# Kernel tuning notes

Hardware: AMD Instinct MI355X
Metric: run time of the kernel (lower is better)

The kernel has to match this reference:

```python
import jax, jax.numpy as jnp
import numpy as np

NUM_USERS, NUM_ITEMS, NUM_GROUPS = 100000, 50000, 20000
D = 64
B, M = 16384, 50


def setup_inputs() -> dict:
    key = jax.random.key(0)
    ks = jax.random.split(key, 16)
    inp = {
        "group_inputs": jax.random.randint(ks[0], (B,), 0, NUM_GROUPS),
        "item_inputs": jax.random.randint(ks[1], (B,), 0, NUM_ITEMS),
        "member_ids": jax.random.randint(ks[2], (B, M), 0, NUM_USERS),
        "member_lengths": jax.random.randint(ks[3], (B,), 0, M),
        # embedding tables (xavier-ish scale)
        "user_table": jax.random.normal(ks[4], (NUM_USERS, D), jnp.float32) * 0.05,
        "item_table": jax.random.normal(ks[5], (NUM_ITEMS, D), jnp.float32) * 0.05,
        "group_table": jax.random.normal(ks[6], (NUM_GROUPS, D), jnp.float32) * 0.05,
        # attention MLP: 2D -> 16 -> 1
        "att_w1": jax.random.normal(ks[7], (2 * D, 16), jnp.float32) * 0.1,
        "att_b1": jnp.zeros((16,), jnp.float32),
        "att_w2": jax.random.normal(ks[8], (16, 1), jnp.float32) * 0.1,
        "att_b2": jnp.zeros((1,), jnp.float32),
        # predict MLP: 3D -> 8 -> 1
        "pred_w1": jax.random.normal(ks[9], (3 * D, 8), jnp.float32) * 0.1,
        "pred_b1": jnp.zeros((8,), jnp.float32),
        "pred_w2": jax.random.normal(ks[10], (8, 1), jnp.float32) * 0.1,
        "pred_b2": jnp.zeros((1,), jnp.float32),
    }
    return inp


def reference(group_inputs, item_inputs, member_ids, member_lengths,
              user_table, item_table, group_table,
              att_w1, att_b1, att_w2, att_b2,
              pred_w1, pred_b1, pred_w2, pred_b2):
    # mask: at least one valid member per group
    mask = jnp.arange(M)[None, :] <= member_lengths[:, None]          # [B, M] bool
    mem_e = user_table[member_ids]                                    # [B, M, D]
    item_e = item_table[item_inputs]                                  # [B, D]

    # attention over members: concat(member, item) -> 16 -> 1
    gi = jnp.concatenate(
        [mem_e, jnp.broadcast_to(item_e[:, None, :], mem_e.shape)], axis=-1)  # [B, M, 2D]
    h = jax.nn.relu(jnp.einsum('bmk,kh->bmh', gi, att_w1) + att_b1)   # [B, M, 16]
    scores = (jnp.einsum('bmh,ho->bmo', h, att_w2) + att_b2)[..., 0]  # [B, M]
    scores = jnp.where(mask, scores, -jnp.inf)
    at_wt = jax.nn.softmax(scores, axis=-1)                           # [B, M]

    g_att = jnp.einsum('bm,bmd->bd', at_wt, mem_e)                    # [B, D]
    g = g_att + group_table[group_inputs]                             # [B, D]

    elem = g * item_e
    new_e = jnp.concatenate([elem, g, item_e], axis=-1)               # [B, 3D]
    ph = jax.nn.relu(new_e @ pred_w1 + pred_b1)                       # [B, 8]
    y = jax.nn.sigmoid(ph @ pred_w2 + pred_b2)                        # [B, 1]
    return y
```

## Files before the change

kernel.cpp:

```cpp
#include <hip/hip_runtime.h>
#include <math.h>

constexpr int MM = 50;
constexpr int DD = 64;
constexpr int HH = 16;
constexpr int PH = 8;
constexpr int WAVES_PER_BLOCK = 4;
constexpr int SLOTS = 56;

__device__ __forceinline__ unsigned bf16rne(float f) {
    const unsigned u = __float_as_uint(f);
    return (u + 0x7FFFu + ((u >> 16) & 1u)) >> 16;
}

__global__ __launch_bounds__(256) void precompute_kernel(
    const float* __restrict__ user_table,
    const float* __restrict__ item_table,
    const int*   __restrict__ item_inputs,
    const float* __restrict__ att_w1,
    const float* __restrict__ att_b1,
    unsigned short* __restrict__ Ubf,
    float* __restrict__ Ib,
    unsigned short* __restrict__ Ub,
    int nU, int B, int userBlocks)
{
    const bool isU = (int)blockIdx.x < userBlocks;
    const float4* rp;
    const float*  w1;
    float acc[HH];
    int row = 0;

    if (isU) {
        row = (int)blockIdx.x * 256 + (int)threadIdx.x;
        if (row >= nU) return;
        rp  = (const float4*)(user_table + (size_t)row * DD);
        w1  = att_w1;
        #pragma unroll
        for (int j = 0; j < HH; ++j) acc[j] = 0.0f;
    } else {
        row = ((int)blockIdx.x - userBlocks) * 256 + (int)threadIdx.x;
        if (row >= B) return;
        const int item = item_inputs[row];
        rp  = (const float4*)(item_table + (size_t)item * DD);
        w1  = att_w1 + (size_t)DD * HH;
        #pragma unroll
        for (int j = 0; j < HH; ++j) acc[j] = att_b1[j];
    }

    unsigned brow[DD / 2];

    #pragma unroll 4
    for (int d4 = 0; d4 < DD / 4; ++d4) {
        const float4 x = rp[d4];
        const float* w = w1 + (size_t)(d4 * 4) * HH;
        #pragma unroll
        for (int j = 0; j < HH; ++j) {
            acc[j] = fmaf(x.x, w[0 * HH + j], acc[j]);
            acc[j] = fmaf(x.y, w[1 * HH + j], acc[j]);
            acc[j] = fmaf(x.z, w[2 * HH + j], acc[j]);
            acc[j] = fmaf(x.w, w[3 * HH + j], acc[j]);
        }
        brow[2 * d4]     = bf16rne(x.x) | (bf16rne(x.y) << 16);
        brow[2 * d4 + 1] = bf16rne(x.z) | (bf16rne(x.w) << 16);
    }

    if (isU) {
        unsigned uw[8];
        #pragma unroll
        for (int w = 0; w < 8; ++w)
            uw[w] = bf16rne(acc[2 * w]) | (bf16rne(acc[2 * w + 1]) << 16);
        uint4* u4 = (uint4*)(Ubf + (size_t)row * HH);
        u4[0] = make_uint4(uw[0], uw[1], uw[2], uw[3]);
        u4[1] = make_uint4(uw[4], uw[5], uw[6], uw[7]);

        uint4* b4 = (uint4*)(Ub + (size_t)row * DD);
        #pragma unroll
        for (int i = 0; i < DD / 8; ++i)
            b4[i] = make_uint4(brow[4 * i], brow[4 * i + 1],
                               brow[4 * i + 2], brow[4 * i + 3]);
    } else {
        float4* o4 = (float4*)(Ib + (size_t)row * HH);
        o4[0] = make_float4(acc[0],  acc[1],  acc[2],  acc[3]);
        o4[1] = make_float4(acc[4],  acc[5],  acc[6],  acc[7]);
        o4[2] = make_float4(acc[8],  acc[9],  acc[10], acc[11]);
        o4[3] = make_float4(acc[12], acc[13], acc[14], acc[15]);
    }
}

__global__ __launch_bounds__(256) void agree_main(
    const int* __restrict__ group_inputs,
    const int* __restrict__ item_inputs,
    const int* __restrict__ member_ids,
    const int* __restrict__ member_lengths,
    const float* __restrict__ item_table,
    const float* __restrict__ group_table,
    const float* __restrict__ att_w2,
    const float* __restrict__ att_b2,
    const float* __restrict__ pred_w1,
    const float* __restrict__ pred_b1,
    const float* __restrict__ pred_w2,
    const float* __restrict__ pred_b2,
    const unsigned short* __restrict__ Ubf,
    const float* __restrict__ Ib,
    const unsigned short* __restrict__ Ub,
    float* __restrict__ out,
    int B)
{
    __shared__ float2 pairs[WAVES_PER_BLOCK][SLOTS];

    const int lane = threadIdx.x & 63;
    const int wv   = threadIdx.x >> 6;
    const int b    = blockIdx.x * WAVES_PER_BLOCK + wv;
    if (b >= B) return;

    const int my_m  = (lane < MM) ? lane : (MM - 1);
    const int my_id = member_ids[b * MM + my_m];
    const int len   = member_lengths[b];
    const int item_idx = item_inputs[b];
    const int gid      = group_inputs[b];

    const float item_d = item_table[(unsigned)(item_idx * DD + lane)];
    const float grp_d  = group_table[(unsigned)(gid * DD + lane)];

    const uint4* up = (const uint4*)(Ubf + ((size_t)(unsigned)my_id * HH));
    const uint4 ua = up[0], ubw = up[1];
    const float* ib = Ib + (size_t)b * HH;

    float score = att_b2[0];
    {
        const unsigned uw[8] = { ua.x, ua.y, ua.z, ua.w,
                                 ubw.x, ubw.y, ubw.z, ubw.w };
        #pragma unroll
        for (int w = 0; w < 8; ++w) {
            const float f0 = __uint_as_float(uw[w] << 16);
            const float f1 = __uint_as_float(uw[w] & 0xFFFF0000u);
            score = fmaf(fmaxf(f0 + ib[2 * w],     0.0f), att_w2[2 * w],     score);
            score = fmaf(fmaxf(f1 + ib[2 * w + 1], 0.0f), att_w2[2 * w + 1], score);
        }
    }

    const bool valid = (lane < MM) && (lane <= len);
    score = valid ? score : -INFINITY;

    float mx = score;
    #pragma unroll
    for (int off = 32; off > 0; off >>= 1) mx = fmaxf(mx, __shfl_xor(mx, off, 64));
    const float e = valid ? __expf(score - mx) : 0.0f;
    float sum = e;
    #pragma unroll
    for (int off = 32; off > 0; off >>= 1) sum += __shfl_xor(sum, off, 64);
    const float wnorm = e / sum;

    if (lane < SLOTS) pairs[wv][lane] = make_float2(wnorm, __int_as_float(my_id));
    __builtin_amdgcn_s_waitcnt(0);

    const int mcnt   = (len < MM - 1 ? len : MM - 1) + 1;
    const int chunks = (mcnt + 7) >> 3;

    float g = 0.0f;
    for (int c = 0; c < chunks; ++c) {
        float2 q[8];
        #pragma unroll
        for (int k = 0; k < 8; ++k) q[k] = pairs[wv][c * 8 + k];
        unsigned short xb[8];
        #pragma unroll
        for (int k = 0; k < 8; ++k) {
            const unsigned idx = (unsigned)(__float_as_int(q[k].y) * DD + lane);
            xb[k] = Ub[idx];
        }
        #pragma unroll
        for (int k = 0; k < 8; ++k)
            g = fmaf(q[k].x, __uint_as_float((unsigned)xb[k] << 16), g);
    }
    g += grp_d;

    const float elem = g * item_d;
    float p[PH];
    {
        const float* pa = pred_w1 + (size_t)lane * PH;
        const float* pb = pred_w1 + (size_t)(DD + lane) * PH;
        const float* pc = pred_w1 + (size_t)(2 * DD + lane) * PH;
        #pragma unroll
        for (int j = 0; j < PH; ++j)
            p[j] = fmaf(elem, pa[j], fmaf(g, pb[j], item_d * pc[j]));
    }
    #pragma unroll
    for (int off = 32; off > 0; off >>= 1) {
        #pragma unroll
        for (int j = 0; j < PH; ++j) p[j] += __shfl_xor(p[j], off, 64);
    }

    if (lane == 0) {
        float acc = pred_b2[0];
        #pragma unroll
        for (int j = 0; j < PH; ++j)
            acc = fmaf(fmaxf(p[j] + pred_b1[j], 0.0f), pred_w2[j], acc);
        out[b] = 1.0f / (1.0f + __expf(-acc));
    }
}

__global__ __launch_bounds__(256) void agree_fallback(
    const int* __restrict__ group_inputs,
    const int* __restrict__ item_inputs,
    const int* __restrict__ member_ids,
    const int* __restrict__ member_lengths,
    const float* __restrict__ user_table,
    const float* __restrict__ item_table,
    const float* __restrict__ group_table,
    const float* __restrict__ att_w1,
    const float* __restrict__ att_b1,
    const float* __restrict__ att_w2,
    const float* __restrict__ att_b2,
    const float* __restrict__ pred_w1,
    const float* __restrict__ pred_b1,
    const float* __restrict__ pred_w2,
    const float* __restrict__ pred_b2,
    float* __restrict__ out,
    int B)
{
    __shared__ float lds_wt[4][MM];
    __shared__ int   lds_id[4][MM];

    const int lane = threadIdx.x & 63;
    const int wave = threadIdx.x >> 6;
    const int b = blockIdx.x * 4 + wave;
    if (b >= B) return;

    const int my_m = (lane < MM) ? lane : (MM - 1);
    const int my_id = member_ids[b * MM + my_m];
    if (lane < MM) lds_id[wave][lane] = my_id;

    const int item_idx = item_inputs[b];
    const float item_d = item_table[(size_t)item_idx * DD + lane];

    float h[HH];
    {
        const float* w1row = att_w1 + (size_t)(DD + lane) * HH;
        #pragma unroll
        for (int j = 0; j < HH; ++j) h[j] = item_d * w1row[j];
        #pragma unroll
        for (int off = 32; off > 0; off >>= 1) {
            #pragma unroll
            for (int j = 0; j < HH; ++j) h[j] += __shfl_xor(h[j], off, 64);
        }
        #pragma unroll
        for (int j = 0; j < HH; ++j) h[j] += att_b1[j];
    }

    const float* myrow = user_table + (size_t)my_id * DD;
    #pragma unroll 4
    for (int d4 = 0; d4 < DD / 4; ++d4) {
        const float4 x = ((const float4*)myrow)[d4];
        const float* w1d = att_w1 + (size_t)(d4 * 4) * HH;
        #pragma unroll
        for (int j = 0; j < HH; ++j) {
            h[j] = fmaf(x.x, w1d[0 * HH + j], h[j]);
            h[j] = fmaf(x.y, w1d[1 * HH + j], h[j]);
            h[j] = fmaf(x.z, w1d[2 * HH + j], h[j]);
            h[j] = fmaf(x.w, w1d[3 * HH + j], h[j]);
        }
    }

    float score = att_b2[0];
    #pragma unroll
    for (int j = 0; j < HH; ++j) score = fmaf(fmaxf(h[j], 0.0f), att_w2[j], score);

    const int len = member_lengths[b];
    const bool valid = (lane < MM) && (lane <= len);
    score = valid ? score : -INFINITY;

    float mx = score;
    #pragma unroll
    for (int off = 32; off > 0; off >>= 1) mx = fmaxf(mx, __shfl_xor(mx, off, 64));
    float e = valid ? __expf(score - mx) : 0.0f;
    float sum = e;
    #pragma unroll
    for (int off = 32; off > 0; off >>= 1) sum += __shfl_xor(sum, off, 64);
    if (lane < MM) lds_wt[wave][lane] = e / sum;
    __builtin_amdgcn_s_waitcnt(0);

    const int mcnt = (len < MM - 1 ? len : MM - 1) + 1;
    float g = 0.0f;
    #pragma unroll 2
    for (int m = 0; m < mcnt; ++m) {
        g = fmaf(lds_wt[wave][m],
                 user_table[(size_t)lds_id[wave][m] * DD + lane], g);
    }
    const int gid = group_inputs[b];
    g += group_table[(size_t)gid * DD + lane];

    const float elem = g * item_d;
    float p[PH];
    {
        const float* pa = pred_w1 + (size_t)lane * PH;
        const float* pb = pred_w1 + (size_t)(DD + lane) * PH;
        const float* pc = pred_w1 + (size_t)(2 * DD + lane) * PH;
        #pragma unroll
        for (int j = 0; j < PH; ++j)
            p[j] = fmaf(elem, pa[j], fmaf(g, pb[j], item_d * pc[j]));
    }
    #pragma unroll
    for (int off = 32; off > 0; off >>= 1) {
        #pragma unroll
        for (int j = 0; j < PH; ++j) p[j] += __shfl_xor(p[j], off, 64);
    }

    if (lane == 0) {
        float acc = pred_b2[0];
        #pragma unroll
        for (int j = 0; j < PH; ++j)
            acc = fmaf(fmaxf(p[j] + pred_b1[j], 0.0f), pred_w2[j], acc);
        out[b] = 1.0f / (1.0f + __expf(-acc));
    }
}

extern "C" void kernel_launch(void* const* d_in, const int* in_sizes, int n_in,
                              void* d_out, int out_size, void* d_ws, size_t ws_size,
                              hipStream_t stream) {
    const int*   group_inputs   = (const int*)d_in[0];
    const int*   item_inputs    = (const int*)d_in[1];
    const int*   member_ids     = (const int*)d_in[2];
    const int*   member_lengths = (const int*)d_in[3];
    const float* user_table     = (const float*)d_in[4];
    const float* item_table     = (const float*)d_in[5];
    const float* group_table    = (const float*)d_in[6];
    const float* att_w1         = (const float*)d_in[7];
    const float* att_b1         = (const float*)d_in[8];
    const float* att_w2         = (const float*)d_in[9];
    const float* att_b2         = (const float*)d_in[10];
    const float* pred_w1        = (const float*)d_in[11];
    const float* pred_b1        = (const float*)d_in[12];
    const float* pred_w2        = (const float*)d_in[13];
    const float* pred_b2        = (const float*)d_in[14];
    float* out = (float*)d_out;

    const int B  = in_sizes[0];
    const int nU = in_sizes[4] / DD;
    const size_t need = (size_t)nU * HH * sizeof(unsigned short)
                      + (size_t)B  * HH * sizeof(float)
                      + (size_t)nU * DD * sizeof(unsigned short);
    const int blocks = (B + WAVES_PER_BLOCK - 1) / WAVES_PER_BLOCK;

    if (ws_size >= need) {
        unsigned short* Ubf = (unsigned short*)d_ws;
        float* Ib = (float*)(Ubf + (size_t)nU * HH);
        unsigned short* Ub = (unsigned short*)(Ib + (size_t)B * HH);
        const int userBlocks = (nU + 255) / 256;
        const int itemBlocks = (B + 255) / 256;
        precompute_kernel<<<userBlocks + itemBlocks, 256, 0, stream>>>(
            user_table, item_table, item_inputs, att_w1, att_b1,
            Ubf, Ib, Ub, nU, B, userBlocks);
        agree_main<<<blocks, 256, 0, stream>>>(
            group_inputs, item_inputs, member_ids, member_lengths,
            item_table, group_table,
            att_w2, att_b2, pred_w1, pred_b1, pred_w2, pred_b2,
            Ubf, Ib, Ub, out, B);
    } else {
        agree_fallback<<<blocks, 256, 0, stream>>>(
            group_inputs, item_inputs, member_ids, member_lengths,
            user_table, item_table, group_table,
            att_w1, att_b1, att_w2, att_b2,
            pred_w1, pred_b1, pred_w2, pred_b2,
            out, B);
    }
}
```

Before: 143.1 us.

## Fuse precompute into single kernel staging member rows as bf16 in LDS

Drops the separate precompute pass that projected the whole user table and wrote bf16 copies to workspace. Each lane now loads its member's fp32 row once, computes the attention hidden layer directly, and stores a bf16 copy into padded LDS. The weighted member sum then reads from LDS instead of re-gathering from global memory. This removes a full-table pass and a second gather, at the cost of more per-lane FMA work and large LDS use that may reduce occupancy.

Measured after the change: 187.9 us. +31.3%, slower.

```diff
diff --git a/kernel.cpp b/kernel.cpp
--- a/kernel.cpp
+++ b/kernel.cpp
@@ -7,199 +7,14 @@
 constexpr int PH = 8;
 constexpr int WAVES_PER_BLOCK = 4;
 constexpr int SLOTS = 56;
+constexpr int USTRIDE = 33;
 
 __device__ __forceinline__ unsigned bf16rne(float f) {
     const unsigned u = __float_as_uint(f);
     return (u + 0x7FFFu + ((u >> 16) & 1u)) >> 16;
 }
 
-__global__ __launch_bounds__(256) void precompute_kernel(
-    const float* __restrict__ user_table,
-    const float* __restrict__ item_table,
-    const int*   __restrict__ item_inputs,
-    const float* __restrict__ att_w1,
-    const float* __restrict__ att_b1,
-    unsigned short* __restrict__ Ubf,
-    float* __restrict__ Ib,
-    unsigned short* __restrict__ Ub,
-    int nU, int B, int userBlocks)
-{
-    const bool isU = (int)blockIdx.x < userBlocks;
-    const float4* rp;
-    const float*  w1;
-    float acc[HH];
-    int row = 0;
-
-    if (isU) {
-        row = (int)blockIdx.x * 256 + (int)threadIdx.x;
-        if (row >= nU) return;
-        rp  = (const float4*)(user_table + (size_t)row * DD);
-        w1  = att_w1;
-        #pragma unroll
-        for (int j = 0; j < HH; ++j) acc[j] = 0.0f;
-    } else {
-        row = ((int)blockIdx.x - userBlocks) * 256 + (int)threadIdx.x;
-        if (row >= B) return;
-        const int item = item_inputs[row];
-        rp  = (const float4*)(item_table + (size_t)item * DD);
-        w1  = att_w1 + (size_t)DD * HH;
-        #pragma unroll
-        for (int j = 0; j < HH; ++j) acc[j] = att_b1[j];
-    }
-
-    unsigned brow[DD / 2];
-
-    #pragma unroll 4
-    for (int d4 = 0; d4 < DD / 4; ++d4) {
-        const float4 x = rp[d4];
-        const float* w = w1 + (size_t)(d4 * 4) * HH;
-        #pragma unroll
-        for (int j = 0; j < HH; ++j) {
-            acc[j] = fmaf(x.x, w[0 * HH + j], acc[j]);
-            acc[j] = fmaf(x.y, w[1 * HH + j], acc[j]);
-            acc[j] = fmaf(x.z, w[2 * HH + j], acc[j]);
-            acc[j] = fmaf(x.w, w[3 * HH + j], acc[j]);
-        }
-        brow[2 * d4]     = bf16rne(x.x) | (bf16rne(x.y) << 16);
-        brow[2 * d4 + 1] = bf16rne(x.z) | (bf16rne(x.w) << 16);
-    }
-
-    if (isU) {
-        unsigned uw[8];
-        #pragma unroll
-        for (int w = 0; w < 8; ++w)
-            uw[w] = bf16rne(acc[2 * w]) | (bf16rne(acc[2 * w + 1]) << 16);
-        uint4* u4 = (uint4*)(Ubf + (size_t)row * HH);
-        u4[0] = make_uint4(uw[0], uw[1], uw[2], uw[3]);
-        u4[1] = make_uint4(uw[4], uw[5], uw[6], uw[7]);
-
-        uint4* b4 = (uint4*)(Ub + (size_t)row * DD);
-        #pragma unroll
-        for (int i = 0; i < DD / 8; ++i)
-            b4[i] = make_uint4(brow[4 * i], brow[4 * i + 1],
-                               brow[4 * i + 2], brow[4 * i + 3]);
-    } else {
-        float4* o4 = (float4*)(Ib + (size_t)row * HH);
-        o4[0] = make_float4(acc[0],  acc[1],  acc[2],  acc[3]);
-        o4[1] = make_float4(acc[4],  acc[5],  acc[6],  acc[7]);
-        o4[2] = make_float4(acc[8],  acc[9],  acc[10], acc[11]);
-        o4[3] = make_float4(acc[12], acc[13], acc[14], acc[15]);
-    }
-}
-
-__global__ __launch_bounds__(256) void agree_main(
-    const int* __restrict__ group_inputs,
-    const int* __restrict__ item_inputs,
-    const int* __restrict__ member_ids,
-    const int* __restrict__ member_lengths,
-    const float* __restrict__ item_table,
-    const float* __restrict__ group_table,
-    const float* __restrict__ att_w2,
-    const float* __restrict__ att_b2,
-    const float* __restrict__ pred_w1,
-    const float* __restrict__ pred_b1,
-    const float* __restrict__ pred_w2,
-    const float* __restrict__ pred_b2,
-    const unsigned short* __restrict__ Ubf,
-    const float* __restrict__ Ib,
-    const unsigned short* __restrict__ Ub,
-    float* __restrict__ out,
-    int B)
-{
-    __shared__ float2 pairs[WAVES_PER_BLOCK][SLOTS];
-
-    const int lane = threadIdx.x & 63;
-    const int wv   = threadIdx.x >> 6;
-    const int b    = blockIdx.x * WAVES_PER_BLOCK + wv;
-    if (b >= B) return;
-
-    const int my_m  = (lane < MM) ? lane : (MM - 1);
-    const int my_id = member_ids[b * MM + my_m];
-    const int len   = member_lengths[b];
-    const int item_idx = item_inputs[b];
-    const int gid      = group_inputs[b];
-
-    const float item_d = item_table[(unsigned)(item_idx * DD + lane)];
-    const float grp_d  = group_table[(unsigned)(gid * DD + lane)];
-
-    const uint4* up = (const uint4*)(Ubf + ((size_t)(unsigned)my_id * HH));
-    const uint4 ua = up[0], ubw = up[1];
-    const float* ib = Ib + (size_t)b * HH;
-
-    float score = att_b2[0];
-    {
-        const unsigned uw[8] = { ua.x, ua.y, ua.z, ua.w,
-                                 ubw.x, ubw.y, ubw.z, ubw.w };
-        #pragma unroll
-        for (int w = 0; w < 8; ++w) {
-            const float f0 = __uint_as_float(uw[w] << 16);
-            const float f1 = __uint_as_float(uw[w] & 0xFFFF0000u);
-            score = fmaf(fmaxf(f0 + ib[2 * w],     0.0f), att_w2[2 * w],     score);
-            score = fmaf(fmaxf(f1 + ib[2 * w + 1], 0.0f), att_w2[2 * w + 1], score);
-        }
-    }
-
-    const bool valid = (lane < MM) && (lane <= len);
-    score = valid ? score : -INFINITY;
-
-    float mx = score;
-    #pragma unroll
-    for (int off = 32; off > 0; off >>= 1) mx = fmaxf(mx, __shfl_xor(mx, off, 64));
-    const float e = valid ? __expf(score - mx) : 0.0f;
-    float sum = e;
-    #pragma unroll
-    for (int off = 32; off > 0; off >>= 1) sum += __shfl_xor(sum, off, 64);
-    const float wnorm = e / sum;
-
-    if (lane < SLOTS) pairs[wv][lane] = make_float2(wnorm, __int_as_float(my_id));
-    __builtin_amdgcn_s_waitcnt(0);
-
-    const int mcnt   = (len < MM - 1 ? len : MM - 1) + 1;
-    const int chunks = (mcnt + 7) >> 3;
-
-    float g = 0.0f;
-    for (int c = 0; c < chunks; ++c) {
-        float2 q[8];
-        #pragma unroll
-        for (int k = 0; k < 8; ++k) q[k] = pairs[wv][c * 8 + k];
-        unsigned short xb[8];
-        #pragma unroll
-        for (int k = 0; k < 8; ++k) {
-            const unsigned idx = (unsigned)(__float_as_int(q[k].y) * DD + lane);
-            xb[k] = Ub[idx];
-        }
-        #pragma unroll
-        for (int k = 0; k < 8; ++k)
-            g = fmaf(q[k].x, __uint_as_float((unsigned)xb[k] << 16), g);
-    }
-    g += grp_d;
-
-    const float elem = g * item_d;
-    float p[PH];
-    {
-        const float* pa = pred_w1 + (size_t)lane * PH;
-        const float* pb = pred_w1 + (size_t)(DD + lane) * PH;
-        const float* pc = pred_w1 + (size_t)(2 * DD + lane) * PH;
-        #pragma unroll
-        for (int j = 0; j < PH; ++j)
-            p[j] = fmaf(elem, pa[j], fmaf(g, pb[j], item_d * pc[j]));
-    }
-    #pragma unroll
-    for (int off = 32; off > 0; off >>= 1) {
-        #pragma unroll
-        for (int j = 0; j < PH; ++j) p[j] += __shfl_xor(p[j], off, 64);
-    }
-
-    if (lane == 0) {
-        float acc = pred_b2[0];
-        #pragma unroll
-        for (int j = 0; j < PH; ++j)
-            acc = fmaf(fmaxf(p[j] + pred_b1[j], 0.0f), pred_w2[j], acc);
-        out[b] = 1.0f / (1.0f + __expf(-acc));
-    }
-}
-
-__global__ __launch_bounds__(256) void agree_fallback(
+__global__ __launch_bounds__(256) void agree_fused(
     const int* __restrict__ group_inputs,
     const int* __restrict__ item_inputs,
     const int* __restrict__ member_ids,
@@ -218,76 +33,95 @@
     float* __restrict__ out,
     int B)
 {
-    __shared__ float lds_wt[4][MM];
-    __shared__ int   lds_id[4][MM];
+    __shared__ unsigned lds_u[WAVES_PER_BLOCK][SLOTS][USTRIDE];
+    __shared__ float    lds_w[WAVES_PER_BLOCK][SLOTS];
 
     const int lane = threadIdx.x & 63;
-    const int wave = threadIdx.x >> 6;
-    const int b = blockIdx.x * 4 + wave;
+    const int wv   = threadIdx.x >> 6;
+    const int b    = blockIdx.x * WAVES_PER_BLOCK + wv;
     if (b >= B) return;
 
-    const int my_m = (lane < MM) ? lane : (MM - 1);
+    const int my_m  = (lane < MM) ? lane : (MM - 1);
     const int my_id = member_ids[b * MM + my_m];
-    if (lane < MM) lds_id[wave][lane] = my_id;
+    const int len      = member_lengths[b];
+    const int item_idx = item_inputs[b];
+    const int gid      = group_inputs[b];
 
-    const int item_idx = item_inputs[b];
     const float item_d = item_table[(size_t)item_idx * DD + lane];
+    const float grp_d  = group_table[(size_t)gid * DD + lane];
 
-    float h[HH];
+    float s[HH];
     {
-        const float* w1row = att_w1 + (size_t)(DD + lane) * HH;
+        const float* w1b = att_w1 + (size_t)(DD + lane) * HH;
         #pragma unroll
-        for (int j = 0; j < HH; ++j) h[j] = item_d * w1row[j];
+        for (int j = 0; j < HH; ++j) s[j] = item_d * w1b[j];
         #pragma unroll
         for (int off = 32; off > 0; off >>= 1) {
             #pragma unroll
-            for (int j = 0; j < HH; ++j) h[j] += __shfl_xor(h[j], off, 64);
+            for (int j = 0; j < HH; ++j) s[j] += __shfl_xor(s[j], off, 64);
         }
         #pragma unroll
-        for (int j = 0; j < HH; ++j) h[j] += att_b1[j];
+        for (int j = 0; j < HH; ++j) s[j] += att_b1[j];
     }
 
-    const float* myrow = user_table + (size_t)my_id * DD;
+    const float4* myrow = (const float4*)(user_table + (size_t)(unsigned)my_id * DD);
     #pragma unroll 4
     for (int d4 = 0; d4 < DD / 4; ++d4) {
-        const float4 x = ((const float4*)myrow)[d4];
-        const float* w1d = att_w1 + (size_t)(d4 * 4) * HH;
+        const float4 x = myrow[d4];
+        const float* w = att_w1 + (size_t)(d4 * 4) * HH;
         #pragma unroll
         for (int j = 0; j < HH; ++j) {
-            h[j] = fmaf(x.x, w1d[0 * HH + j], h[j]);
-            h[j] = fmaf(x.y, w1d[1 * HH + j], h[j]);
-            h[j] = fmaf(x.z, w1d[2 * HH + j], h[j]);
-            h[j] = fmaf(x.w, w1d[3 * HH + j], h[j]);
+            s[j] = fmaf(x.x, w[0 * HH + j], s[j]);
+            s[j] = fmaf(x.y, w[1 * HH + j], s[j]);
+            s[j] = fmaf(x.z, w[2 * HH + j], s[j]);
+            s[j] = fmaf(x.w, w[3 * HH + j], s[j]);
+        }
+        if (lane < SLOTS) {
+            lds_u[wv][lane][2 * d4]     = bf16rne(x.x) | (bf16rne(x.y) << 16);
+            lds_u[wv][lane][2 * d4 + 1] = bf16rne(x.z) | (bf16rne(x.w) << 16);
         }
     }
 
     float score = att_b2[0];
     #pragma unroll
-    for (int j = 0; j < HH; ++j) score = fmaf(fmaxf(h[j], 0.0f), att_w2[j], score);
+    for (int j = 0; j < HH; ++j)
+        score = fmaf(fmaxf(s[j], 0.0f), att_w2[j], score);
 
-    const int len = member_lengths[b];
     const bool valid = (lane < MM) && (lane <= len);
     score = valid ? score : -INFINITY;
 
     float mx = score;
     #pragma unroll
     for (int off = 32; off > 0; off >>= 1) mx = fmaxf(mx, __shfl_xor(mx, off, 64));
-    float e = valid ? __expf(score - mx) : 0.0f;
+    const float e = valid ? __expf(score - mx) : 0.0f;
     float sum = e;
     #pragma unroll
     for (int off = 32; off > 0; off >>= 1) sum += __shfl_xor(sum, off, 64);
-    if (lane < MM) lds_wt[wave][lane] = e / sum;
+    const float wnorm = e / sum;
+
+    if (lane < SLOTS) lds_w[wv][lane] = wnorm;
     __builtin_amdgcn_s_waitcnt(0);
 
-    const int mcnt = (len < MM - 1 ? len : MM - 1) + 1;
+    const int mcnt   = (len < MM - 1 ? len : MM - 1) + 1;
+    const int chunks = (mcnt + 7) >> 3;
+    const int half   = lane >> 1;
+    const unsigned oddmask = (lane & 1) ? 0u : 0xFFFFu;
+
     float g = 0.0f;
-    #pragma unroll 2
-    for (int m = 0; m < mcnt; ++m) {
-        g = fmaf(lds_wt[wave][m],
-                 user_table[(size_t)lds_id[wave][m] * DD + lane], g);
+    for (int c = 0; c < chunks; ++c) {
+        float    w8[8];
+        unsigned u8[8];
+        #pragma unroll
+        for (int k = 0; k < 8; ++k) w8[k] = lds_w[wv][c * 8 + k];
+        #pragma unroll
+        for (int k = 0; k < 8; ++k) u8[k] = lds_u[wv][c * 8 + k][half];
+        #pragma unroll
+        for (int k = 0; k < 8; ++k) {
+            const unsigned hb = (lane & 1) ? (u8[k] & 0xFFFF0000u) : (u8[k] << 16);
+            g = fmaf(w8[k], __uint_as_float(hb), g);
+        }
     }
-    const int gid = group_inputs[b];
-    g += group_table[(size_t)gid * DD + lane];
+    g += grp_d;
 
     const float elem = g * item_d;
     float p[PH];
@@ -334,33 +168,14 @@
     const float* pred_b2        = (const float*)d_in[14];
     float* out = (float*)d_out;
 
-    const int B  = in_sizes[0];
-    const int nU = in_sizes[4] / DD;
-    const size_t need = (size_t)nU * HH * sizeof(unsigned short)
-                      + (size_t)B  * HH * sizeof(float)
-                      + (size_t)nU * DD * sizeof(unsigned short);
+    const int B = in_sizes[0];
+    (void)d_ws; (void)ws_size;
+
     const int blocks = (B + WAVES_PER_BLOCK - 1) / WAVES_PER_BLOCK;
-
-    if (ws_size >= need) {
-        unsigned short* Ubf = (unsigned short*)d_ws;
-        float* Ib = (float*)(Ubf + (size_t)nU * HH);
-        unsigned short* Ub = (unsigned short*)(Ib + (size_t)B * HH);
-        const int userBlocks = (nU + 255) / 256;
-        const int itemBlocks = (B + 255) / 256;
-        precompute_kernel<<<userBlocks + itemBlocks, 256, 0, stream>>>(
-            user_table, item_table, item_inputs, att_w1, att_b1,
-            Ubf, Ib, Ub, nU, B, userBlocks);
-        agree_main<<<blocks, 256, 0, stream>>>(
-            group_inputs, item_inputs, member_ids, member_lengths,
-            item_table, group_table,
-            att_w2, att_b2, pred_w1, pred_b1, pred_w2, pred_b2,
-            Ubf, Ib, Ub, out, B);
-    } else {
-        agree_fallback<<<blocks, 256, 0, stream>>>(
-            group_inputs, item_inputs, member_ids, member_lengths,
-            user_table, item_table, group_table,
-            att_w1, att_b1, att_w2, att_b2,
-            pred_w1, pred_b1, pred_w2, pred_b2,
-            out, B);
-    }
+    agree_fused<<<blocks, 256, 0, stream>>>(
+        group_inputs, item_inputs, member_ids, member_lengths,
+        user_table, item_table, group_table,
+        att_w1, att_b1, att_w2, att_b2,
+        pred_w1, pred_b1, pred_w2, pred_b2,
+        out, B);
 }
```

## Gather member bf16 rows with 16-byte loads split across lane groups

Applied to the files above, without the earlier changes.

Reworks the weighted member-row gather. Each group of 8 lanes now fetches one member's 64-element bf16 row using 16-byte vector loads, and all 7 chunks (56 slots) are loaded unconditionally. Before, the loop issued 2-byte per-lane loads and was bounded by the member length. Per-lane partial sums are then reduced with cross-lane shuffles and redistributed through shared memory. The aim is fewer, wider memory transactions and more loads in flight, at the cost of fetching rows for masked members (weight zero) and an extra shuffle reduction plus an LDS round trip.

New measurement: 144.5 us. Within noise of the previous version (+1.0%).

```diff
diff --git a/kernel.cpp b/kernel.cpp
--- a/kernel.cpp
+++ b/kernel.cpp
@@ -6,7 +6,8 @@
 constexpr int HH = 16;
 constexpr int PH = 8;
 constexpr int WAVES_PER_BLOCK = 4;
-constexpr int SLOTS = 56;
+constexpr int SLOTS  = 56;
+constexpr int CHUNKS = 7;
 
 __device__ __forceinline__ unsigned bf16rne(float f) {
     const unsigned u = __float_as_uint(f);
@@ -107,6 +108,7 @@
     int B)
 {
     __shared__ float2 pairs[WAVES_PER_BLOCK][SLOTS];
+    __shared__ float  gbuf[WAVES_PER_BLOCK][DD];
 
     const int lane = threadIdx.x & 63;
     const int wv   = threadIdx.x >> 6;
@@ -115,7 +117,7 @@
 
     const int my_m  = (lane < MM) ? lane : (MM - 1);
     const int my_id = member_ids[b * MM + my_m];
-    const int len   = member_lengths[b];
+    const int len      = member_lengths[b];
     const int item_idx = item_inputs[b];
     const int gid      = group_inputs[b];
 
@@ -154,25 +156,48 @@
     if (lane < SLOTS) pairs[wv][lane] = make_float2(wnorm, __int_as_float(my_id));
     __builtin_amdgcn_s_waitcnt(0);
 
-    const int mcnt   = (len < MM - 1 ? len : MM - 1) + 1;
-    const int chunks = (mcnt + 7) >> 3;
-
-    float g = 0.0f;
-    for (int c = 0; c < chunks; ++c) {
-        float2 q[8];
-        #pragma unroll
-        for (int k = 0; k < 8; ++k) q[k] = pairs[wv][c * 8 + k];
-        unsigned short xb[8];
-        #pragma unroll
-        for (int k = 0; k < 8; ++k) {
-            const unsigned idx = (unsigned)(__float_as_int(q[k].y) * DD + lane);
-            xb[k] = Ub[idx];
-        }
-        #pragma unroll
-        for (int k = 0; k < 8; ++k)
-            g = fmaf(q[k].x, __uint_as_float((unsigned)xb[k] << 16), g);
-    }
-    g += grp_d;
+    const int i = lane >> 3;
+    const int j = lane & 7;
+
+    float2 pr[CHUNKS];
+    #pragma unroll
+    for (int c = 0; c < CHUNKS; ++c) pr[c] = pairs[wv][c * 8 + i];
+
+    uint4 r4[CHUNKS];
+    #pragma unroll
+    for (int c = 0; c < CHUNKS; ++c) {
+        const unsigned row = (unsigned)__float_as_int(pr[c].y);
+        r4[c] = *(const uint4*)(Ub + (size_t)row * DD + (j << 3));
+    }
+
+    float gp[8];
+    #pragma unroll
+    for (int r = 0; r < 8; ++r) gp[r] = 0.0f;
+    #pragma unroll
+    for (int c = 0; c < CHUNKS; ++c) {
+        const float w = pr[c].x;
+        const unsigned wd[4] = { r4[c].x, r4[c].y, r4[c].z, r4[c].w };
+        #pragma unroll
+        for (int t = 0; t < 4; ++t) {
+            gp[2 * t]     = fmaf(w, __uint_as_float(wd[t] << 16),         gp[2 * t]);
+            gp[2 * t + 1] = fmaf(w, __uint_as_float(wd[t] & 0xFFFF0000u), gp[2 * t + 1]);
+        }
+    }
+
+    #pragma unroll
+    for (int off = 8; off < 64; off <<= 1) {
+        #pragma unroll
+        for (int r = 0; r < 8; ++r) gp[r] += __shfl_xor(gp[r], off, 64);
+    }
+
+    if (lane < 8) {
+        float4* g4 = (float4*)&gbuf[wv][lane * 8];
+        g4[0] = make_float4(gp[0], gp[1], gp[2], gp[3]);
+        g4[1] = make_float4(gp[4], gp[5], gp[6], gp[7]);
+    }
+    __builtin_amdgcn_s_waitcnt(0);
+
+    const float g = gbuf[wv][lane] + grp_d;
 
     const float elem = g * item_d;
     float p[PH];
@@ -181,20 +206,20 @@
         const float* pb = pred_w1 + (size_t)(DD + lane) * PH;
         const float* pc = pred_w1 + (size_t)(2 * DD + lane) * PH;
         #pragma unroll
-        for (int j = 0; j < PH; ++j)
-            p[j] = fmaf(elem, pa[j], fmaf(g, pb[j], item_d * pc[j]));
+        for (int jj = 0; jj < PH; ++jj)
+            p[jj] = fmaf(elem, pa[jj], fmaf(g, pb[jj], item_d * pc[jj]));
     }
     #pragma unroll
     for (int off = 32; off > 0; off >>= 1) {
         #pragma unroll
-        for (int j = 0; j < PH; ++j) p[j] += __shfl_xor(p[j], off, 64);
+        for (int jj = 0; jj < PH; ++jj) p[jj] += __shfl_xor(p[jj], off, 64);
     }
 
     if (lane == 0) {
         float acc = pred_b2[0];
         #pragma unroll
-        for (int j = 0; j < PH; ++j)
-            acc = fmaf(fmaxf(p[j] + pred_b1[j], 0.0f), pred_w2[j], acc);
+        for (int jj = 0; jj < PH; ++jj)
+            acc = fmaf(fmaxf(p[jj] + pred_b1[jj], 0.0f), pred_w2[jj], acc);
         out[b] = 1.0f / (1.0f + __expf(-acc));
     }
 }
```
